# Performance work log

Measured on AMD Instinct MI355X. Metric: run time of the kernel, lower is better.

The kernel has to match this reference:

```python
import jax, jax.numpy as jnp
import numpy as np

B, T, C, H = 128, 256, 256, 8
HS = C // H  # 32
EPS = 1e-5


def _layernorm(x, g, b):
    mu = jnp.mean(x, axis=-1, keepdims=True)
    var = jnp.mean(jnp.square(x - mu), axis=-1, keepdims=True)
    return g * (x - mu) / jnp.sqrt(var + EPS) + b


def setup_inputs() -> dict:
    key = jax.random.key(0)
    ks = jax.random.split(key, 12)
    s = 0.02
    return {
        "x": jax.random.normal(ks[0], (B, T, C), dtype=jnp.float32),
        "Wk": jax.random.normal(ks[1], (H, C, HS), dtype=jnp.float32) * s,
        "Wq": jax.random.normal(ks[2], (H, C, HS), dtype=jnp.float32) * s,
        "Wv": jax.random.normal(ks[3], (H, C, HS), dtype=jnp.float32) * s,
        "Wp": jax.random.normal(ks[4], (C, C), dtype=jnp.float32) * s,
        "bp": jnp.zeros((C,), dtype=jnp.float32),
        "W1": jax.random.normal(ks[5], (C, 4 * C), dtype=jnp.float32) * s,
        "b1": jnp.zeros((4 * C,), dtype=jnp.float32),
        "W2": jax.random.normal(ks[6], (4 * C, C), dtype=jnp.float32) * s,
        "b2": jnp.zeros((C,), dtype=jnp.float32),
        "g1": jnp.ones((C,), dtype=jnp.float32),
        "be1": jnp.zeros((C,), dtype=jnp.float32),
        "g2": jnp.ones((C,), dtype=jnp.float32),
        "be2": jnp.zeros((C,), dtype=jnp.float32),
    }


def reference(x, Wk, Wq, Wv, Wp, bp, W1, b1, W2, b2, g1, be1, g2, be2):
    Bx, Tx, Cx = x.shape
    # --- multi-head self-attention on ln1(x) ---
    h = _layernorm(x, g1, be1)
    k = jnp.einsum('btc,hcd->bhtd', h, Wk)
    q = jnp.einsum('btc,hcd->bhtd', h, Wq)
    v = jnp.einsum('btc,hcd->bhtd', h, Wv)
    # NOTE: source computes k @ q^T (transposed vs standard) and scales by C**-0.5
    scores = jnp.einsum('bhtd,bhsd->bhts', k, q) * (Cx ** -0.5)
    mask = jnp.tril(jnp.ones((Tx, Tx), dtype=bool))  # causal lower-triangular
    scores = jnp.where(mask, scores, -jnp.inf)
    w = jax.nn.softmax(scores, axis=-1)
    o = jnp.einsum('bhts,bhsd->bhtd', w, v)
    o = o.transpose(0, 2, 1, 3).reshape(Bx, Tx, Cx)  # concat heads
    x = x + (o @ Wp + bp)
    # --- feed-forward (swish) on ln2(x) ---
    h2 = _layernorm(x, g2, be2)
    f = h2 @ W1 + b1
    f = f * jax.nn.sigmoid(f)  # swish
    f = f @ W2 + b2
    return x + f
```

## Files before the change

### kernel.cpp

```cpp
#include <hip/hip_runtime.h>
#include <cstdint>

#define BB 128
#define TT 256
#define CC 256
#define HH 8
#define HSZ 32
#define NT (BB*TT)
#define CF (4*CC)
#define LN_EPS 1e-5f
#define SCALE 0.0625f

typedef __attribute__((ext_vector_type(8))) __bf16 bf16x8;
typedef __attribute__((ext_vector_type(4))) float f32x4;
typedef __attribute__((ext_vector_type(16))) float f32x16;
typedef __attribute__((ext_vector_type(2))) long i64x2;
typedef unsigned short u16;
typedef unsigned int u32;
typedef unsigned char u8;

__device__ __forceinline__ u16 f2bf(float f) {
  u32 u = __float_as_uint(f);
  u32 r = (u + 0x7fffu + ((u >> 16) & 1u)) >> 16;
  return (u16)r;
}
__device__ __forceinline__ u8 f2f8(float f) {
  return (u8)(__builtin_amdgcn_cvt_pk_fp8_f32(f, f, 0, false) & 0xff);
}
__device__ __forceinline__ u32 f2f8x4(float a, float b, float c, float d) {
  u32 pk = (u32)__builtin_amdgcn_cvt_pk_fp8_f32(a, b, 0, false);
  return (u32)__builtin_amdgcn_cvt_pk_fp8_f32(c, d, (int)pk, true);
}
__device__ __forceinline__ uint2 f2bfx4(float a, float b, float c, float d) {
  uint2 r;
  asm("v_cvt_pk_bf16_f32 %0, %1, %2" : "=v"(r.x) : "v"(a), "v"(b));
  asm("v_cvt_pk_bf16_f32 %0, %1, %2" : "=v"(r.y) : "v"(c), "v"(d));
  return r;
}
__device__ __forceinline__ int swz3i(int r) { return (r ^ (r >> 2)) & 3; }
__device__ __forceinline__ int pkrow(int row, int k) {
  int g = (k >> 4) & 3, h = (k >> 3) & 1, j = k & 7;
  int c = (h << 1) + (g >> 1);
  int cp = c ^ swz3i(row);
  return (k & ~63) + cp * 16 + ((g & 1) << 3) + j;
}

__device__ __forceinline__ void gload16(const void* g, void* l) {
  __builtin_amdgcn_global_load_lds(
      (const __attribute__((address_space(1))) u32*)(uintptr_t)g,
      (__attribute__((address_space(3))) u32*)(u32)(uintptr_t)l,
      16, 0, 0);
}

__device__ __forceinline__ void wait_vm0() {
  asm volatile("s_waitcnt vmcnt(0)" ::: "memory");
  __builtin_amdgcn_sched_barrier(0);
}
__device__ __forceinline__ void wait_vm4() {
  asm volatile("s_waitcnt vmcnt(4)" ::: "memory");
  __builtin_amdgcn_sched_barrier(0);
}
__device__ __forceinline__ void wait_vm8() {
  asm volatile("s_waitcnt vmcnt(8)" ::: "memory");
  __builtin_amdgcn_sched_barrier(0);
}
__device__ __forceinline__ void wait_vm4_lgkm0() {
  asm volatile("s_waitcnt vmcnt(4) lgkmcnt(0)" ::: "memory");
  __builtin_amdgcn_sched_barrier(0);
}
__device__ __forceinline__ void wait_vm0_lgkm0() {
  asm volatile("s_waitcnt vmcnt(0) lgkmcnt(0)" ::: "memory");
  __builtin_amdgcn_sched_barrier(0);
}
__device__ __forceinline__ void sbar() {
  __builtin_amdgcn_s_barrier();
  __builtin_amdgcn_sched_barrier(0);
}

__global__ __launch_bounds__(256) void conv_t(
    const float* __restrict__ Wk, const float* __restrict__ Wq,
    const float* __restrict__ Wv, const float* __restrict__ Wp,
    const float* __restrict__ W1, const float* __restrict__ W2,
    u8* __restrict__ WkqvT8, u8* __restrict__ WpT8,
    u8* __restrict__ W1T8, u8* __restrict__ W2T8) {
  __shared__ u8 ldsT[64][68];
  int bid = blockIdx.x, tid = threadIdx.x;
  int n0, k0, K;
  u8* dst;
  int mode;
  const float* src = nullptr;
  int sk = 0;
  if (bid < 48) {
    mode = 0; n0 = (bid >> 2) * 64; k0 = (bid & 3) * 64; K = 256; dst = WkqvT8;
  } else if (bid < 112) {
    int l = bid - 48;
    mode = 1; n0 = (l >> 2) * 64; k0 = (l & 3) * 64; K = 256; dst = W1T8;
    src = W1; sk = 1024;
  } else if (bid < 176) {
    int l = bid - 112;
    mode = 1; n0 = (l >> 4) * 64; k0 = (l & 15) * 64; K = 1024; dst = W2T8;
    src = W2; sk = 256;
  } else {
    int l = bid - 176;
    mode = 1; n0 = (l >> 2) * 64; k0 = (l & 3) * 64; K = 256; dst = WpT8;
    src = Wp; sk = 256;
  }
  int kr = tid >> 2;
  int nbase = (tid & 3) * 16;
#pragma unroll
  for (int u = 0; u < 4; ++u) {
    int nl = nbase + u * 4;
    int ng = n0 + nl;
    float4 v;
    if (mode == 0) {
      const float* W = (ng < 256) ? Wk : (ng < 512 ? Wq : Wv);
      int inner = ng & 255;
      v = *reinterpret_cast<const float4*>(
          &W[((inner >> 5) << 13) + (size_t)(k0 + kr) * 32 + (inner & 31)]);
    } else {
      v = *reinterpret_cast<const float4*>(
          &src[(size_t)(k0 + kr) * sk + ng]);
    }
    ldsT[nl + 0][kr] = f2f8(v.x);
    ldsT[nl + 1][kr] = f2f8(v.y);
    ldsT[nl + 2][kr] = f2f8(v.z);
    ldsT[nl + 3][kr] = f2f8(v.w);
  }
  __syncthreads();
  int nl = tid >> 2;
  int nglob = n0 + nl;
  int sz = swz3i(nglob);
  u8* drow = dst + (size_t)nglob * K + k0;
#pragma unroll
  for (int c4 = (tid & 3) * 4; c4 < (tid & 3) * 4 + 4; ++c4) {
    int q = c4 >> 1, s = c4 & 1;
    int kb = q * 8 + s * 4;
    u32 pk = (u32)ldsT[nl][kb] | ((u32)ldsT[nl][kb + 1] << 8) |
             ((u32)ldsT[nl][kb + 2] << 16) | ((u32)ldsT[nl][kb + 3] << 24);
    int g = (kb >> 4) & 3, h8 = (kb >> 3) & 1;
    int cp = ((h8 << 1) + (g >> 1)) ^ sz;
    *reinterpret_cast<u32*>(drow + cp * 16 + ((g & 1) << 3) + (kb & 7)) = pk;
  }
}

__global__ __launch_bounds__(256) void ln_kernel(const float* __restrict__ x,
                                                 const float* __restrict__ g,
                                                 const float* __restrict__ b,
                                                 u8* __restrict__ out) {
  int tid = threadIdx.x;
  int wid = tid >> 6, lane = tid & 63;
  int row = blockIdx.x * 4 + wid;
  const float4 v = reinterpret_cast<const float4*>(x + (size_t)row * CC)[lane];
  float s = v.x + v.y + v.z + v.w;
#pragma unroll
  for (int o = 32; o; o >>= 1) s += __shfl_xor(s, o, 64);
  float mu = s * (1.0f / CC);
  float dx = v.x - mu, dy = v.y - mu, dz = v.z - mu, dw = v.w - mu;
  float ss = dx * dx + dy * dy + dz * dz + dw * dw;
#pragma unroll
  for (int o = 32; o; o >>= 1) ss += __shfl_xor(ss, o, 64);
  float inv = rsqrtf(ss * (1.0f / CC) + LN_EPS);
  const float4 gv = reinterpret_cast<const float4*>(g)[lane];
  const float4 bv = reinterpret_cast<const float4*>(b)[lane];
  u32 pk = f2f8x4(gv.x * dx * inv + bv.x, gv.y * dy * inv + bv.y,
                  gv.z * dz * inv + bv.z, gv.w * dw * inv + bv.w);
  *reinterpret_cast<u32*>(out + (size_t)row * CC + pkrow(row, lane * 4)) = pk;
}

template <int EPI>
__device__ __forceinline__ void epi_store(f32x4 v, int m, int n,
                                          const float* bias,
                                          const float* resid, void* outp,
                                          int N) {
  size_t off = (size_t)m * N + n;
  if (EPI == 0) {
    u16 pk[4];
#pragma unroll
    for (int r = 0; r < 4; ++r) pk[r] = f2bf(v[r]);
    *reinterpret_cast<uint2*>(&((u16*)outp)[off]) = *reinterpret_cast<uint2*>(pk);
  } else if (EPI == 1) {
    const float4 bv = *reinterpret_cast<const float4*>(&bias[n]);
    const float4 rv = *reinterpret_cast<const float4*>(&resid[off]);
    float4 o;
    o.x = v[0] + bv.x + rv.x;
    o.y = v[1] + bv.y + rv.y;
    o.z = v[2] + bv.z + rv.z;
    o.w = v[3] + bv.w + rv.w;
    *reinterpret_cast<float4*>(&((float*)outp)[off]) = o;
  }
}

template <int NB, int EPI>
__global__ __launch_bounds__(512, 4) void panel_fused(
    const u8* __restrict__ Asrc, const u8* __restrict__ WT8,
    const float* __restrict__ bias, const float* __restrict__ resid,
    void* __restrict__ outp, int N) {
  __shared__ u8 Bw[4][256][64];
  int tid = threadIdx.x;
  int w = tid >> 6, lane = tid & 63;
  int l32 = lane & 31, h = lane >> 5;
  int th = w >> 2, fq = w & 3;
  int m0 = blockIdx.x * 64;

#define STAGEP(nb)                                                            \
  {                                                                           \
    _Pragma("unroll") for (int it = 0; it < 8; ++it) {                        \
      int f = it * 512 + tid;                                                 \
      int kg = f >> 10, t = (f >> 2) & 255, c = f & 3;                        \
      gload16(WT8 + (size_t)((nb) * 256 + t) * 256 + kg * 64 + c * 16,        \
              &Bw[0][0][0] + f * 16);                                         \
    }                                                                         \
  }
  i64x2 aa[4][2];
  {
    int ar = th * 32 + l32;
    int az = swz3i(ar);
#pragma unroll
    for (int kg = 0; kg < 4; ++kg)
#pragma unroll
      for (int p = 0; p < 2; ++p)
        aa[kg][p] = *reinterpret_cast<const i64x2*>(
            Asrc + (size_t)(m0 + ar) * 256 + kg * 64 +
            ((((h << 1) + p) ^ az) << 4));
  }
  STAGEP(0);

#pragma unroll 1
  for (int nb = 0; nb < NB; ++nb) {
    if (nb == 0) wait_vm0(); else wait_vm8();
    sbar();
    f32x16 a1[2] = {};
#pragma unroll
    for (int kg = 0; kg < 4; ++kg) {
#pragma unroll
      for (int p = 0; p < 2; ++p) {
        i64x2 bB[2];
#pragma unroll
        for (int j = 0; j < 2; ++j) {
          int br = fq * 64 + j * 32 + l32, bz = swz3i(br);
          bB[j] = *reinterpret_cast<const i64x2*>(
              &Bw[kg][br][(((h << 1) + p) ^ bz) << 4]);
        }
#pragma unroll
        for (int j = 0; j < 2; ++j) {
          a1[j] = __builtin_amdgcn_mfma_f32_32x32x16_fp8_fp8(
              bB[j][0], aa[kg][p][0], a1[j], 0, 0, 0);
          a1[j] = __builtin_amdgcn_mfma_f32_32x32x16_fp8_fp8(
              bB[j][1], aa[kg][p][1], a1[j], 0, 0, 0);
        }
      }
    }
    sbar();
    if (nb < NB - 1) STAGEP(nb + 1);
    int m = m0 + th * 32 + l32;
#pragma unroll
    for (int j = 0; j < 2; ++j) {
#pragma unroll
      for (int q = 0; q < 4; ++q) {
        int n = nb * 256 + fq * 64 + j * 32 + q * 8 + h * 4;
        f32x4 v = {a1[j][q * 4 + 0], a1[j][q * 4 + 1],
                   a1[j][q * 4 + 2], a1[j][q * 4 + 3]};
        epi_store<EPI>(v, m, n, bias, resid, outp, N);
      }
    }
  }
#undef STAGEP
}

__global__ __launch_bounds__(512, 4) void ffn_fused(
    const u8* __restrict__ hb, const u8* __restrict__ W1T8,
    const u8* __restrict__ W2T8, const float* __restrict__ b1,
    const float* __restrict__ b2, const float* __restrict__ x2,
    float* __restrict__ outp) {
  __shared__ u8 Bw1[4][128][64];
  __shared__ u8 Bw2[2][256][64];
  __shared__ u8 Ff[2][64][64];
  __shared__ float b1l[1024];
  int tid = threadIdx.x;
  int w = tid >> 6, lane = tid & 63;
  int l32 = lane & 31, h = lane >> 5;
  int th = w >> 2, fq = w & 3;
  int m0 = blockIdx.x * 64;

#define STAGE_W1(nb)                                                          \
  {                                                                           \
    _Pragma("unroll") for (int it = 0; it < 4; ++it) {                        \
      int f = it * 512 + tid;                                                 \
      int kg = f >> 9, t = (f >> 2) & 127, c = f & 3;                         \
      gload16(W1T8 + (size_t)((nb) * 128 + t) * 256 + kg * 64 + c * 16,       \
              &Bw1[0][0][0] + f * 16);                                        \
    }                                                                         \
  }
#define STAGE_W2(nb)                                                          \
  {                                                                           \
    _Pragma("unroll") for (int it = 0; it < 4; ++it) {                        \
      int f = it * 512 + tid;                                                 \
      int kg2 = f >> 10, o = (f >> 2) & 255, c = f & 3;                       \
      gload16(W2T8 + (size_t)o * 1024 + (nb) * 128 + kg2 * 64 + c * 16,       \
              &Bw2[0][0][0] + f * 16);                                        \
    }                                                                         \
  }
  i64x2 aa[4][2];
  {
    int ar = th * 32 + l32;
    int az = swz3i(ar);
#pragma unroll
    for (int kg = 0; kg < 4; ++kg)
#pragma unroll
      for (int p = 0; p < 2; ++p)
        aa[kg][p] = *reinterpret_cast<const i64x2*>(
            hb + (size_t)(m0 + ar) * 256 + kg * 64 +
            ((((h << 1) + p) ^ az) << 4));
  }
  if (w < 4) gload16(b1 + (size_t)(w * 256 + lane * 4), b1l + w * 256 + lane * 4);
  STAGE_W1(0);
  STAGE_W2(0);

  f32x16 acc2[2] = {};
#pragma unroll 1
  for (int nb = 0; nb < 8; ++nb) {
    wait_vm4();
    sbar();
    f32x16 a1 = {};
#pragma unroll
    for (int kg = 0; kg < 4; ++kg) {
      int br = fq * 32 + l32, bz = swz3i(br);
#pragma unroll
      for (int p = 0; p < 2; ++p) {
        i64x2 bB = *reinterpret_cast<const i64x2*>(
            &Bw1[kg][br][(((h << 1) + p) ^ bz) << 4]);
        a1 = __builtin_amdgcn_mfma_f32_32x32x16_fp8_fp8(
            bB[0], aa[kg][p][0], a1, 0, 0, 0);
        a1 = __builtin_amdgcn_mfma_f32_32x32x16_fp8_fp8(
            bB[1], aa[kg][p][1], a1, 0, 0, 0);
      }
    }
    sbar();
    if (nb < 7) STAGE_W1(nb + 1);
    int kg2w = fq >> 1;
    {
      int t = th * 32 + l32;
      int tz = swz3i(t);
#pragma unroll
      for (int q = 0; q < 4; ++q) {
        int g = (fq & 1) * 2 + (q >> 1);
        int hh = q & 1;
        int c = (hh << 1) + (g >> 1);
        const float4 bv = *reinterpret_cast<const float4*>(
            &b1l[nb * 128 + fq * 32 + q * 8 + h * 4]);
        float bf[4] = {bv.x, bv.y, bv.z, bv.w};
        float sv[4];
#pragma unroll
        for (int r = 0; r < 4; ++r) {
          float fv = a1[q * 4 + r] + bf[r];
          float e = __builtin_amdgcn_exp2f(fv * -1.44269504f);
          sv[r] = fv * __builtin_amdgcn_rcpf(1.0f + e);
        }
        *reinterpret_cast<u32*>(
            &Ff[kg2w][t][((c ^ tz) << 4) + ((g & 1) << 3) + h * 4]) =
            f2f8x4(sv[0], sv[1], sv[2], sv[3]);
      }
    }
    if (nb < 7) wait_vm4_lgkm0();
    else        wait_vm0_lgkm0();
    sbar();
#pragma unroll
    for (int kg2 = 0; kg2 < 2; ++kg2)
#pragma unroll
      for (int p = 0; p < 2; ++p) {
        int ar2 = th * 32 + l32;
        i64x2 fa = *reinterpret_cast<const i64x2*>(
            &Ff[kg2][ar2][(((h << 1) + p) ^ swz3i(ar2)) << 4]);
        i64x2 bb2[2];
#pragma unroll
        for (int j = 0; j < 2; ++j) {
          int br = fq * 64 + j * 32 + l32;
          bb2[j] = *reinterpret_cast<const i64x2*>(
              &Bw2[kg2][br][(((h << 1) + p) ^ swz3i(br)) << 4]);
        }
#pragma unroll
        for (int j = 0; j < 2; ++j) {
          acc2[j] = __builtin_amdgcn_mfma_f32_32x32x16_fp8_fp8(
              bb2[j][0], fa[0], acc2[j], 0, 0, 0);
          acc2[j] = __builtin_amdgcn_mfma_f32_32x32x16_fp8_fp8(
              bb2[j][1], fa[1], acc2[j], 0, 0, 0);
        }
      }
    sbar();
    if (nb < 7) STAGE_W2(nb + 1);
  }
#undef STAGE_W1
#undef STAGE_W2
  int m = m0 + th * 32 + l32;
#pragma unroll
  for (int j = 0; j < 2; ++j) {
#pragma unroll
    for (int q = 0; q < 4; ++q) {
      int n = fq * 64 + j * 32 + q * 8 + h * 4;
      f32x4 v = {acc2[j][q * 4 + 0], acc2[j][q * 4 + 1],
                 acc2[j][q * 4 + 2], acc2[j][q * 4 + 3]};
      epi_store<1>(v, m, n, b2, x2, outp, CC);
    }
  }
}

__global__ __launch_bounds__(256) void attn_kernel(const u16* __restrict__ kqv,
                                                   u8* __restrict__ o8) {
  __shared__ u16 q_lds[256 * 32];
  __shared__ u16 vT[32 * 256];
  __shared__ u16 pT[4 * 16 * 64];
  int bh = blockIdx.x;
  int b = bh >> 3, h = bh & 7;
  int tid = threadIdx.x, wid = tid >> 6, lane = tid & 63;
  int l16 = lane & 15, lh = lane >> 4;
  const size_t rowbase = (size_t)b * TT * 768;
  {
    int sr = tid >> 2, c = tid & 3;
    for (int s = sr; s < 256; s += 64) {
      uint4 qv = *reinterpret_cast<const uint4*>(
          &kqv[rowbase + (size_t)s * 768 + 256 + h * 32 + c * 8]);
      *reinterpret_cast<uint4*>((char*)q_lds + ((s * 64 + c * 16) ^ ((s & 7) << 4))) = qv;
      u16 tmp[8];
      *reinterpret_cast<uint4*>(tmp) = *reinterpret_cast<const uint4*>(
          &kqv[rowbase + (size_t)s * 768 + 512 + h * 32 + c * 8]);
#pragma unroll
      for (int dd = 0; dd < 8; ++dd) {
        int e = dd ^ c;
        int d = c * 8 + e;
        vT[d * 256 + (((s >> 3) ^ (d & 7)) << 3) + (s & 7)] = tmp[e];
      }
    }
  }
  __syncthreads();
  u16* pw = &pT[wid * 16 * 64];
  const float C1 = 0.09016844f;
  for (int j = 0; j < 4; ++j) {
    int t16 = (j * 4 + wid) * 16;
    bf16x8 kb = *reinterpret_cast<const bf16x8*>(
        &kqv[rowbase + (size_t)(t16 + l16) * 768 + h * 32 + lh * 8]);
    float m2 = -3e38f, lsum = 0.f;
    f32x4 oacc[2] = {};
    for (int st = 0; st <= j; ++st) {
      int s0 = st << 6;
      float v[4][4];
      float pm[4];
#pragma unroll
      for (int sj = 0; sj < 4; ++sj) {
        int srow = s0 + sj * 16 + l16;
        bf16x8 qa = *reinterpret_cast<const bf16x8*>(
            (char*)q_lds + ((srow * 64 + lh * 16) ^ ((srow & 7) << 4)));
        f32x4 z = {0.f, 0.f, 0.f, 0.f};
        f32x4 sc = __builtin_amdgcn_mfma_f32_16x16x32_bf16(qa, kb, z, 0, 0, 0);
#pragma unroll
        for (int r = 0; r < 4; ++r) {
          float val = sc[r];
          if (st == j) {
            if (sj * 16 + lh * 4 + r > wid * 16 + l16) val = -3e38f;
          }
          v[sj][r] = val;
        }
        pm[sj] = fmaxf(fmaxf(v[sj][0], v[sj][1]), fmaxf(v[sj][2], v[sj][3]));
      }
      float mx = fmaxf(fmaxf(pm[0], pm[1]), fmaxf(pm[2], pm[3]));
      mx = fmaxf(mx, __shfl_xor(mx, 16, 64));
      mx = fmaxf(mx, __shfl_xor(mx, 32, 64));
      float mxs = mx * C1;
      if (!__all(mxs <= m2 + 8.0f)) {
        float mn = fmaxf(m2, mxs);
        float alpha = exp2f(m2 - mn);
        m2 = mn;
        lsum *= alpha;
#pragma unroll
        for (int r = 0; r < 4; ++r) {
          float a = __shfl(alpha, (lane & 48) | (lh * 4 + r), 64);
          oacc[0][r] *= a;
          oacc[1][r] *= a;
        }
      }
#pragma unroll
      for (int sj = 0; sj < 4; ++sj) {
        float p0 = exp2f(__builtin_fmaf(v[sj][0], C1, -m2));
        float p1 = exp2f(__builtin_fmaf(v[sj][1], C1, -m2));
        float p2 = exp2f(__builtin_fmaf(v[sj][2], C1, -m2));
        float p3 = exp2f(__builtin_fmaf(v[sj][3], C1, -m2));
        lsum += (p0 + p1) + (p2 + p3);
        uint2 pkv = f2bfx4(p0, p1, p2, p3);
        *reinterpret_cast<uint2*>(
            (char*)pw + ((l16 * 128 + sj * 32 + lh * 8) ^ ((l16 & 7) << 4))) = pkv;
      }
#pragma unroll
      for (int ks = 0; ks < 2; ++ks) {
        bf16x8 pa = *reinterpret_cast<const bf16x8*>(
            (char*)pw + ((l16 * 128 + ks * 64 + lh * 16) ^ ((l16 & 7) << 4)));
#pragma unroll
        for (int nI = 0; nI < 2; ++nI) {
          int d = nI * 16 + l16;
          int sch = ((s0 + ks * 32 + lh * 8) >> 3) ^ (d & 7);
          bf16x8 vb = *reinterpret_cast<const bf16x8*>(&vT[d * 256 + (sch << 3)]);
          oacc[nI] = __builtin_amdgcn_mfma_f32_16x16x32_bf16(pa, vb, oacc[nI], 0, 0, 0);
        }
      }
    }
    lsum += __shfl_xor(lsum, 16, 64);
    lsum += __shfl_xor(lsum, 32, 64);
#pragma unroll
    for (int r = 0; r < 4; ++r) {
      float ls = __shfl(lsum, (lane & 48) | (lh * 4 + r), 64);
      float inv = 1.0f / ls;
      int t = t16 + lh * 4 + r;
      size_t rb = (size_t)(b * TT + t) * CC;
#pragma unroll
      for (int nI = 0; nI < 2; ++nI) {
        int c = h * HSZ + nI * 16 + l16;
        o8[rb + pkrow(t, c)] = f2f8(oacc[nI][r] * inv);
      }
    }
  }
}

extern "C" void kernel_launch(void* const* d_in, const int* in_sizes, int n_in,
                              void* d_out, int out_size, void* d_ws, size_t ws_size,
                              hipStream_t stream) {
  const float* x   = (const float*)d_in[0];
  const float* Wk  = (const float*)d_in[1];
  const float* Wq  = (const float*)d_in[2];
  const float* Wv  = (const float*)d_in[3];
  const float* Wp  = (const float*)d_in[4];
  const float* bp  = (const float*)d_in[5];
  const float* W1  = (const float*)d_in[6];
  const float* b1  = (const float*)d_in[7];
  const float* W2  = (const float*)d_in[8];
  const float* b2  = (const float*)d_in[9];
  const float* g1  = (const float*)d_in[10];
  const float* be1 = (const float*)d_in[11];
  const float* g2  = (const float*)d_in[12];
  const float* be2 = (const float*)d_in[13];

  char* ws = (char*)d_ws;
  u16* kqv = (u16*)(ws + 0);
  u8*  o8  = (u8*)(ws + 50331648);
  float* x2 = (float*)(ws + 67108864);
  u8*  hb  = (u8*)(ws + 100663296);
  char* wb = ws + 117440512;
  u8*  WkqvT8 = (u8*)(wb);
  u8*  WpT8   = (u8*)(wb + 196608);
  u8*  W1T8   = (u8*)(wb + 196608 + 65536);
  u8*  W2T8   = (u8*)(wb + 196608 + 65536 + 262144);

  conv_t<<<192, 256, 0, stream>>>(Wk, Wq, Wv, Wp, W1, W2,
                                  WkqvT8, WpT8, W1T8, W2T8);
  ln_kernel<<<NT / 4, 256, 0, stream>>>(x, g1, be1, hb);
  panel_fused<3, 0><<<NT / 64, 512, 0, stream>>>(
      hb, WkqvT8, nullptr, nullptr, kqv, 768);
  attn_kernel<<<BB * HH, 256, 0, stream>>>(kqv, o8);
  panel_fused<1, 1><<<NT / 64, 512, 0, stream>>>(
      o8, WpT8, bp, x, x2, 256);
  ln_kernel<<<NT / 4, 256, 0, stream>>>(x2, g2, be2, hb);
  ffn_fused<<<NT / 64, 512, 0, stream>>>(hb, W1T8, W2T8, b1, b2, x2, (float*)d_out);
}
```

Baseline: 144.8 us.

## Fuse second layernorm into projection epilogue and widen attention blocks to 512 threads

The output-projection GEMM epilogue now computes the residual sum, stores x2, then reduces per-row sum and sum-of-squares across the four column-quarter waves through shared memory. It writes the fp8 layernorm output directly, which removes the separate ln_kernel launch and its re-read of x2. Separately, the attention kernel uses 8 waves instead of 4, each handling two query tiles instead of four, for more parallelism per block. The variance is computed as E[x^2]-mu^2, which is less numerically robust, and the larger attention block may reduce occupancy.

```diff
diff --git a/kernel.cpp b/kernel.cpp
--- a/kernel.cpp
+++ b/kernel.cpp
@@ -194,8 +194,11 @@
 __global__ __launch_bounds__(512, 4) void panel_fused(
     const u8* __restrict__ Asrc, const u8* __restrict__ WT8,
     const float* __restrict__ bias, const float* __restrict__ resid,
-    void* __restrict__ outp, int N) {
+    void* __restrict__ outp, int N,
+    const float* __restrict__ gamma, const float* __restrict__ beta,
+    u8* __restrict__ out8) {
   __shared__ u8 Bw[4][256][64];
+  __shared__ float red[4][64][2];
   int tid = threadIdx.x;
   int w = tid >> 6, lane = tid & 63;
   int l32 = lane & 31, h = lane >> 5;
@@ -252,15 +255,63 @@
     }
     sbar();
     if (nb < NB - 1) STAGEP(nb + 1);
+
     int m = m0 + th * 32 + l32;
-#pragma unroll
-    for (int j = 0; j < 2; ++j) {
-#pragma unroll
-      for (int q = 0; q < 4; ++q) {
-        int n = nb * 256 + fq * 64 + j * 32 + q * 8 + h * 4;
-        f32x4 v = {a1[j][q * 4 + 0], a1[j][q * 4 + 1],
-                   a1[j][q * 4 + 2], a1[j][q * 4 + 3]};
-        epi_store<EPI>(v, m, n, bias, resid, outp, N);
+    if (EPI == 2) {
+      float s1 = 0.f, s2 = 0.f;
+#pragma unroll
+      for (int j = 0; j < 2; ++j) {
+#pragma unroll
+        for (int q = 0; q < 4; ++q) {
+          int n = fq * 64 + j * 32 + q * 8 + h * 4;
+          size_t off = (size_t)m * 256 + n;
+          const float4 bv = *reinterpret_cast<const float4*>(&bias[n]);
+          const float4 rv = *reinterpret_cast<const float4*>(&resid[off]);
+          float4 o;
+          o.x = a1[j][q * 4 + 0] + bv.x + rv.x;
+          o.y = a1[j][q * 4 + 1] + bv.y + rv.y;
+          o.z = a1[j][q * 4 + 2] + bv.z + rv.z;
+          o.w = a1[j][q * 4 + 3] + bv.w + rv.w;
+          *reinterpret_cast<float4*>(&((float*)outp)[off]) = o;
+          a1[j][q * 4 + 0] = o.x; a1[j][q * 4 + 1] = o.y;
+          a1[j][q * 4 + 2] = o.z; a1[j][q * 4 + 3] = o.w;
+          s1 += (o.x + o.y) + (o.z + o.w);
+          s2 += (o.x * o.x + o.y * o.y) + (o.z * o.z + o.w * o.w);
+        }
+      }
+      s1 += __shfl_xor(s1, 32, 64);
+      s2 += __shfl_xor(s2, 32, 64);
+      if (h == 0) { red[fq][th * 32 + l32][0] = s1; red[fq][th * 32 + l32][1] = s2; }
+      sbar();
+      int tl = th * 32 + l32;
+      float S1 = (red[0][tl][0] + red[1][tl][0]) + (red[2][tl][0] + red[3][tl][0]);
+      float S2 = (red[0][tl][1] + red[1][tl][1]) + (red[2][tl][1] + red[3][tl][1]);
+      float mu = S1 * (1.0f / 256.0f);
+      float inv = rsqrtf(S2 * (1.0f / 256.0f) - mu * mu + LN_EPS);
+#pragma unroll
+      for (int j = 0; j < 2; ++j) {
+#pragma unroll
+        for (int q = 0; q < 4; ++q) {
+          int n = fq * 64 + j * 32 + q * 8 + h * 4;
+          const float4 gv = *reinterpret_cast<const float4*>(&gamma[n]);
+          const float4 bb = *reinterpret_cast<const float4*>(&beta[n]);
+          u32 pk = f2f8x4(gv.x * (a1[j][q * 4 + 0] - mu) * inv + bb.x,
+                          gv.y * (a1[j][q * 4 + 1] - mu) * inv + bb.y,
+                          gv.z * (a1[j][q * 4 + 2] - mu) * inv + bb.z,
+                          gv.w * (a1[j][q * 4 + 3] - mu) * inv + bb.w);
+          *reinterpret_cast<u32*>(out8 + (size_t)m * 256 + pkrow(m, n)) = pk;
+        }
+      }
+    } else {
+#pragma unroll
+      for (int j = 0; j < 2; ++j) {
+#pragma unroll
+        for (int q = 0; q < 4; ++q) {
+          int n = nb * 256 + fq * 64 + j * 32 + q * 8 + h * 4;
+          f32x4 v = {a1[j][q * 4 + 0], a1[j][q * 4 + 1],
+                     a1[j][q * 4 + 2], a1[j][q * 4 + 3]};
+          epi_store<EPI>(v, m, n, bias, resid, outp, N);
+        }
       }
     }
   }
@@ -404,11 +455,11 @@
   }
 }
 
-__global__ __launch_bounds__(256) void attn_kernel(const u16* __restrict__ kqv,
+__global__ __launch_bounds__(512) void attn_kernel(const u16* __restrict__ kqv,
                                                    u8* __restrict__ o8) {
   __shared__ u16 q_lds[256 * 32];
   __shared__ u16 vT[32 * 256];
-  __shared__ u16 pT[4 * 16 * 64];
+  __shared__ u16 pT[8 * 16 * 64];
   int bh = blockIdx.x;
   int b = bh >> 3, h = bh & 7;
   int tid = threadIdx.x, wid = tid >> 6, lane = tid & 63;
@@ -416,7 +467,8 @@
   const size_t rowbase = (size_t)b * TT * 768;
   {
     int sr = tid >> 2, c = tid & 3;
-    for (int s = sr; s < 256; s += 64) {
+#pragma unroll
+    for (int s = sr; s < 256; s += 128) {
       uint4 qv = *reinterpret_cast<const uint4*>(
           &kqv[rowbase + (size_t)s * 768 + 256 + h * 32 + c * 8]);
       *reinterpret_cast<uint4*>((char*)q_lds + ((s * 64 + c * 16) ^ ((s & 7) << 4))) = qv;
@@ -434,13 +486,16 @@
   __syncthreads();
   u16* pw = &pT[wid * 16 * 64];
   const float C1 = 0.09016844f;
-  for (int j = 0; j < 4; ++j) {
-    int t16 = (j * 4 + wid) * 16;
+#pragma unroll
+  for (int jj = 0; jj < 2; ++jj) {
+    int ti = jj * 8 + wid;
+    int t16 = ti * 16;
+    int stmax = ti >> 2;
     bf16x8 kb = *reinterpret_cast<const bf16x8*>(
         &kqv[rowbase + (size_t)(t16 + l16) * 768 + h * 32 + lh * 8]);
     float m2 = -3e38f, lsum = 0.f;
     f32x4 oacc[2] = {};
-    for (int st = 0; st <= j; ++st) {
+    for (int st = 0; st <= stmax; ++st) {
       int s0 = st << 6;
       float v[4][4];
       float pm[4];
@@ -454,8 +509,8 @@
 #pragma unroll
         for (int r = 0; r < 4; ++r) {
           float val = sc[r];
-          if (st == j) {
-            if (sj * 16 + lh * 4 + r > wid * 16 + l16) val = -3e38f;
+          if (st == stmax) {
+            if (sj * 16 + lh * 4 + r > (ti & 3) * 16 + l16) val = -3e38f;
           }
           v[sj][r] = val;
         }
@@ -551,10 +606,9 @@
                                   WkqvT8, WpT8, W1T8, W2T8);
   ln_kernel<<<NT / 4, 256, 0, stream>>>(x, g1, be1, hb);
   panel_fused<3, 0><<<NT / 64, 512, 0, stream>>>(
-      hb, WkqvT8, nullptr, nullptr, kqv, 768);
-  attn_kernel<<<BB * HH, 256, 0, stream>>>(kqv, o8);
-  panel_fused<1, 1><<<NT / 64, 512, 0, stream>>>(
-      o8, WpT8, bp, x, x2, 256);
-  ln_kernel<<<NT / 4, 256, 0, stream>>>(x2, g2, be2, hb);
+      hb, WkqvT8, nullptr, nullptr, kqv, 768, nullptr, nullptr, nullptr);
+  attn_kernel<<<BB * HH, 512, 0, stream>>>(kqv, o8);
+  panel_fused<1, 2><<<NT / 64, 512, 0, stream>>>(
+      o8, WpT8, bp, x, x2, 256, g2, be2, hb);
   ffn_fused<<<NT / 64, 512, 0, stream>>>(hb, W1T8, W2T8, b1, b2, x2, (float*)d_out);
 }
```

Measured after the change: 136.4 us. -5.8%, faster.
